# Optimization experiments

Hardware: AMD Instinct MI355X
Metric: run time of the kernel (lower is better)

## Reference

```python
import jax, jax.numpy as jnp
import numpy as np

L, D, H, DH, DI, V, S, B = 12, 768, 12, 64, 3072, 32000, 512, 2
LN_EPS = 1e-3  # keras LayerNormalization default epsilon

def _gelu(x):
    return x * 0.5 * (1.0 + jnp.tanh(np.sqrt(2.0 / np.pi).astype(np.float32) * (x + 0.044715 * x ** 3)))

def _layer_norm(x, g, b):
    mu = jnp.mean(x, axis=-1, keepdims=True)
    var = jnp.mean((x - mu) ** 2, axis=-1, keepdims=True)
    return (x - mu) * jax.lax.rsqrt(var + LN_EPS) * g + b

def _rel_shift(x, klen):
    # x: [qlen, rlen, b, n] -> shifted [qlen, klen, b, n]
    q, r, b, n = x.shape
    x = x.reshape(r, q, b, n)[1:].reshape(q, r - 1, b, n)
    return x[:, :klen]

def _pos_emb():
    # relative positions klen..-qlen+1 (attn_type='bi', mems=None -> klen=qlen=S)
    pos_seq = jnp.arange(S, -S, -1.0, dtype=jnp.float32)                      # [2S]
    inv_freq = 1.0 / (10000.0 ** (jnp.arange(0, D, 2, dtype=jnp.float32) / D))
    sinusoid = pos_seq[:, None] * inv_freq[None, :]
    pe = jnp.concatenate([jnp.sin(sinusoid), jnp.cos(sinusoid)], axis=-1)     # [2S, D]
    return jnp.broadcast_to(pe[:, None, :], (2 * S, B, D))                    # [2S, B, D]

def setup_inputs() -> dict:
    key = jax.random.key(0)
    ks = jax.random.split(key, 12)
    rn = lambda k, sh: 0.02 * jax.random.normal(k, sh, dtype=jnp.float32)
    return {
        "inp_k": jax.random.randint(ks[0], (S, B), 0, V),
        "seg_ids": jax.random.randint(ks[1], (S, B), 0, 2),
        "input_mask": jax.random.randint(ks[2], (S, B), 0, 2),
        "lookup_table": rn(ks[3], (V, D)),
        "Wq": rn(ks[4], (L, D, H, DH)),
        "Wk": rn(ks[5], (L, D, H, DH)),
        "Wv": rn(ks[6], (L, D, H, DH)),
        "Wr": rn(ks[7], (L, D, H, DH)),
        "Wo": rn(ks[8], (L, D, H, DH)),
        "r_w_bias": rn(ks[9], (L, H, DH)),
        "r_r_bias": rn(ks[10], (L, H, DH)),
        "r_s_bias": rn(ks[11], (L, H, DH)),
        "seg_embed": rn(jax.random.fold_in(key, 100), (L, 2, H, DH)),
        "ln_attn_g": jnp.ones((L, D), jnp.float32),
        "ln_attn_b": jnp.zeros((L, D), jnp.float32),
        "ln_ff_g": jnp.ones((L, D), jnp.float32),
        "ln_ff_b": jnp.zeros((L, D), jnp.float32),
        "ff_w1": rn(jax.random.fold_in(key, 101), (L, D, DI)),
        "ff_b1": jnp.zeros((L, DI), jnp.float32),
        "ff_w2": rn(jax.random.fold_in(key, 102), (L, DI, D)),
        "ff_b2": jnp.zeros((L, D), jnp.float32),
    }

def reference(inp_k, seg_ids, input_mask, lookup_table, Wq, Wk, Wv, Wr, Wo,
              r_w_bias, r_r_bias, r_s_bias, seg_embed,
              ln_attn_g, ln_attn_b, ln_ff_g, ln_ff_b,
              ff_w1, ff_b1, ff_w2, ff_b2):
    h = lookup_table[inp_k]                                                   # [S,B,D]
    r = _pos_emb()                                                            # [2S,B,D]
    # segment "same/different" one-hot matrix [q,k,b,2]
    seg_mat = jax.nn.one_hot((seg_ids[:, None, :] != seg_ids[None, :, :]).astype(jnp.int32), 2, dtype=jnp.float32)
    attn_mask = input_mask.astype(jnp.float32)[None, :, :, None]              # [1,S,B,1] broadcast over q,heads
    scale = DH ** -0.5
    for l in range(L):
        q = jnp.einsum('ibh,hnd->ibnd', h, Wq[l])
        k = jnp.einsum('ibh,hnd->ibnd', h, Wk[l])
        v = jnp.einsum('ibh,hnd->ibnd', h, Wv[l])
        kr = jnp.einsum('ibh,hnd->ibnd', r, Wr[l])                            # [2S,B,n,d]
        ac = jnp.einsum('ibnd,jbnd->ijbn', q + r_w_bias[l], k)
        bd = _rel_shift(jnp.einsum('ibnd,jbnd->ijbn', q + r_r_bias[l], kr), S)
        ef = jnp.einsum('ibnd,snd->ibns', q + r_s_bias[l], seg_embed[l])
        ef = jnp.einsum('ijbs,ibns->ijbn', seg_mat, ef)
        score = (ac + bd + ef) * scale - 1e30 * attn_mask
        prob = jax.nn.softmax(score, axis=1)                                  # softmax over key axis j
        vec = jnp.einsum('ijbn,jbnd->ibnd', prob, v)
        h = _layer_norm(jnp.einsum('ibnd,hnd->ibh', vec, Wo[l]) + h, ln_attn_g[l], ln_attn_b[l])
        ff = _gelu(jnp.einsum('ibd,df->ibf', h, ff_w1[l]) + ff_b1[l])
        ff = jnp.einsum('ibf,fd->ibd', ff, ff_w2[l]) + ff_b2[l]
        h = _layer_norm(ff + h, ln_ff_g[l], ln_ff_b[l])
    return h
```

## Files before the change

### kernel.cpp

```cpp
#include <hip/hip_runtime.h>
#include <hip/hip_bf16.h>
#include <math.h>

#define S 512
#define B 2
#define D 768
#define H 12
#define DH 64
#define DI 3072
#define NL 12
#define NTOK (S * B)

typedef __attribute__((ext_vector_type(8))) short short8v;
typedef __attribute__((ext_vector_type(4))) float f32x4;

__device__ __forceinline__ unsigned short f2b(float f) {
  union { float f; unsigned int u; } v; v.f = f;
  unsigned int r = v.u + 0x7fffu + ((v.u >> 16) & 1u);
  return (unsigned short)(r >> 16);
}
__device__ __forceinline__ float b2f(unsigned short u) {
  union { unsigned int u; float f; } v; v.u = ((unsigned int)u) << 16;
  return v.f;
}

__device__ __forceinline__ float gelu_f(float x) {
  const float c = 0.7978845608028654f;
  float t = tanhf(c * (x + 0.044715f * x * x * x));
  return x * 0.5f * (1.0f + t);
}

__device__ __forceinline__ int vkey(int r) {
  return (((r & 7) ^ ((r >> 3) & 7)) << 3);
}

__global__ __launch_bounds__(256) void embed_kernel(const int* __restrict__ inp_k,
                                                    const float* __restrict__ lut,
                                                    float* __restrict__ h,
                                                    unsigned short* __restrict__ h_bf) {
  int t = blockIdx.x;
  int id = inp_k[t];
  for (int j = threadIdx.x; j < D; j += 256) {
    float v = lut[(size_t)id * D + j];
    h[t * D + j] = v;
    h_bf[t * D + j] = f2b(v);
  }
}

__global__ __launch_bounds__(384) void posemb_kernel(unsigned short* __restrict__ r2b) {
  int j = blockIdx.x;
  int d = threadIdx.x;
  float pos = (float)(S - j);
  float inv_freq = expf(-logf(10000.0f) * (2.0f * (float)d / (float)D));
  float x = pos * inv_freq;
  r2b[j * D + d]       = f2b(sinf(x));
  r2b[j * D + 384 + d] = f2b(cosf(x));
}

__device__ __forceinline__ void transpose_swz(const float* __restrict__ src,
                                              unsigned short* __restrict__ dst,
                                              int K, int N, int tile, int n_base,
                                              unsigned short* __restrict__ Ls ) {
  int ntk = K >> 6;
  int tk = tile % ntk, tn = tile / ntk;
  int k0 = tk << 6, n0 = tn << 6;
  int tid = threadIdx.x;
  int kk = tid >> 4, c4 = (tid & 15) * 4;
#pragma unroll
  for (int r = 0; r < 4; ++r) {
    int k = kk + r * 16;
    float4 a = *(const float4*)&src[(size_t)(k0 + k) * N + n0 + c4];
    Ls[(c4 + 0) * 72 + k] = f2b(a.x);
    Ls[(c4 + 1) * 72 + k] = f2b(a.y);
    Ls[(c4 + 2) * 72 + k] = f2b(a.z);
    Ls[(c4 + 3) * 72 + k] = f2b(a.w);
  }
  __syncthreads();
  int nl = tid >> 2, kc0 = (tid & 3) << 4;
  int ng = n_base + n0;
  size_t tilebase = ((size_t)(ng >> 7) * ntk + tk) * 8192;
  int row = (ng & 64) + nl;
  int key = (row & 7) << 3;
  short8v v0 = *(short8v*)&Ls[nl * 72 + kc0];
  short8v v1 = *(short8v*)&Ls[nl * 72 + kc0 + 8];
  *(short8v*)&dst[tilebase + row * 64 + (kc0 ^ key)] = v0;
  *(short8v*)&dst[tilebase + row * 64 + ((kc0 + 8) ^ key)] = v1;
}

__global__ __launch_bounds__(256) void prep_all(const float* __restrict__ Wq,
                                                const float* __restrict__ Wk,
                                                const float* __restrict__ Wv,
                                                const float* __restrict__ Wr,
                                                const float* __restrict__ Wo,
                                                const float* __restrict__ W1,
                                                const float* __restrict__ W2,
                                                unsigned short* __restrict__ wqkv_t,
                                                unsigned short* __restrict__ wr_t,
                                                unsigned short* __restrict__ wo_t,
                                                unsigned short* __restrict__ w1_t,
                                                unsigned short* __restrict__ w2_t) {
  __shared__ __align__(16) unsigned short Ls[64 * 72];
  const size_t DD = (size_t)D * D;
  const size_t DDI = (size_t)D * DI;
  int tb = blockIdx.x;
  int l = tb / 1872, t2 = tb % 1872;
  int tid = threadIdx.x;
  if (t2 < 432) {
    int which = t2 / 144, tile = t2 % 144;
    const float* src = (which == 0 ? Wq : (which == 1 ? Wk : Wv)) + l * DD;
    transpose_swz(src, wqkv_t + l * 3 * DD, D, D, tile, which * D, Ls);
  } else if (t2 < 576) {
    transpose_swz(Wr + l * DD, wr_t + l * DD, D, D, t2 - 432, 0, Ls);
  } else if (t2 < 1152) {
    transpose_swz(W1 + l * DDI, w1_t + l * DDI, D, DI, t2 - 576, 0, Ls);
  } else if (t2 < 1728) {
    transpose_swz(W2 + l * DDI, w2_t + l * DDI, DI, D, t2 - 1152, 0, Ls);
  } else {
    int c = t2 - 1728;
    int tkk = c % 12, tnn = c / 12;
    int k0 = tkk << 6, n0 = tnn << 6;
    int nl = tid >> 2, kc0 = (tid & 3) << 4;
    const float* srcp = Wo + l * DD + (size_t)(n0 + nl) * D + k0 + kc0;
    float4 a0 = *(const float4*)&srcp[0];
    float4 a1 = *(const float4*)&srcp[4];
    float4 a2 = *(const float4*)&srcp[8];
    float4 a3 = *(const float4*)&srcp[12];
    short8v v0, v1;
    v0[0] = (short)f2b(a0.x); v0[1] = (short)f2b(a0.y); v0[2] = (short)f2b(a0.z); v0[3] = (short)f2b(a0.w);
    v0[4] = (short)f2b(a1.x); v0[5] = (short)f2b(a1.y); v0[6] = (short)f2b(a1.z); v0[7] = (short)f2b(a1.w);
    v1[0] = (short)f2b(a2.x); v1[1] = (short)f2b(a2.y); v1[2] = (short)f2b(a2.z); v1[3] = (short)f2b(a2.w);
    v1[4] = (short)f2b(a3.x); v1[5] = (short)f2b(a3.y); v1[6] = (short)f2b(a3.z); v1[7] = (short)f2b(a3.w);
    unsigned short* dst = wo_t + l * DD;
    size_t tilebase = ((size_t)(n0 >> 7) * 12 + tkk) * 8192;
    int row = (n0 & 64) + nl;
    int key = (row & 7) << 3;
    *(short8v*)&dst[tilebase + row * 64 + (kc0 ^ key)] = v0;
    *(short8v*)&dst[tilebase + row * 64 + ((kc0 + 8) ^ key)] = v1;
  }
}

template <int ACT, int OUTBF>
__device__ __forceinline__ void gemm_tile(const unsigned short* __restrict__ A,
                                          const unsigned short* __restrict__ Wt,
                                          const float* __restrict__ bias,
                                          float* __restrict__ Cf,
                                          unsigned short* __restrict__ Cb,
                                          int N, int K, int bm, int bn,
                                          int kbeg, int kend) {
  __shared__ __align__(16) unsigned short As[64 * 64];
  __shared__ __align__(16) unsigned short Bs[128 * 64];
  const int tid = threadIdx.x, lane = tid & 63, w = tid >> 6;
  const int l8 = lane >> 3, lm8 = lane & 7;
  const int aColByte = ((lm8 ^ l8) << 4);
  const int KT = K >> 6;
  const size_t wtn = (size_t)(bn >> 7) * KT;

  f32x4 acc[4][2];
#pragma unroll
  for (int mi = 0; mi < 4; ++mi)
#pragma unroll
    for (int ni = 0; ni < 2; ++ni)
      acc[mi][ni] = (f32x4){0.f, 0.f, 0.f, 0.f};

  for (int kt = kbeg; kt < kend; kt += 64) {
    __syncthreads();
#pragma unroll
    for (int c = 0; c < 2; ++c) {
      int row = c * 32 + w * 8 + l8;
      const char* src = (const char*)&A[(size_t)(bm + row) * K + kt] + aColByte;
      __builtin_amdgcn_global_load_lds(
          (const __attribute__((address_space(1))) void*)src,
          (__attribute__((address_space(3))) void*)((char*)As + c * 4096 + w * 1024),
          16, 0, 0);
    }
    const char* wt = (const char*)&Wt[(wtn + (kt >> 6)) * 8192];
#pragma unroll
    for (int c = 0; c < 4; ++c) {
      __builtin_amdgcn_global_load_lds(
          (const __attribute__((address_space(1))) void*)(wt + c * 4096 + w * 1024 + lane * 16),
          (__attribute__((address_space(3))) void*)((char*)Bs + c * 4096 + w * 1024),
          16, 0, 0);
    }
    __syncthreads();
#pragma unroll
    for (int ks = 0; ks < 2; ++ks) {
      const int kus = ks * 32 + (lane >> 4) * 8;
      short8v af[4], bf[2];
#pragma unroll
      for (int mi = 0; mi < 4; ++mi) {
        int row = mi * 16 + (lane & 15);
        af[mi] = *(const short8v*)&As[row * 64 + (kus ^ ((row & 7) << 3))];
      }
#pragma unroll
      for (int ni = 0; ni < 2; ++ni) {
        int row = w * 32 + ni * 16 + (lane & 15);
        bf[ni] = *(const short8v*)&Bs[row * 64 + (kus ^ ((row & 7) << 3))];
      }
#pragma unroll
      for (int mi = 0; mi < 4; ++mi)
#pragma unroll
        for (int ni = 0; ni < 2; ++ni)
          acc[mi][ni] = __builtin_amdgcn_mfma_f32_16x16x32_bf16(af[mi], bf[ni], acc[mi][ni], 0, 0, 0);
    }
  }

  int r0 = (lane >> 4) * 4, cc = lane & 15;
#pragma unroll
  for (int mi = 0; mi < 4; ++mi) {
    int row = bm + mi * 16 + r0;
#pragma unroll
    for (int ni = 0; ni < 2; ++ni) {
      int col = bn + w * 32 + ni * 16 + cc;
      float bv = bias ? bias[col] : 0.0f;
#pragma unroll
      for (int r = 0; r < 4; ++r) {
        float v = acc[mi][ni][r] + bv;
        if (ACT == 1) v = gelu_f(v);
        if (OUTBF) Cb[(size_t)(row + r) * N + col] = f2b(v);
        else       Cf[(size_t)(row + r) * N + col] = v;
      }
    }
  }
}

__global__ __launch_bounds__(256) void gemm_qkvkr(const unsigned short* __restrict__ h_bf,
                                                  const unsigned short* __restrict__ wqkv,
                                                  const unsigned short* __restrict__ r2_bf,
                                                  const unsigned short* __restrict__ wr,
                                                  unsigned short* __restrict__ qkv_bf,
                                                  unsigned short* __restrict__ kr_bf) {
  int bx = blockIdx.x;
  const unsigned short *A, *W;
  unsigned short* C;
  int N, bm, bn;
  if (bx < 288) {
    A = h_bf; W = wqkv; C = qkv_bf; N = 2304;
    bm = (bx / 18) * 64; bn = (bx % 18) * 128;
  } else {
    int b2 = bx - 288;
    A = r2_bf; W = wr; C = kr_bf; N = 768;
    bm = (b2 / 6) * 64; bn = (b2 % 6) * 128;
  }
  gemm_tile<0, 1>(A, W, nullptr, nullptr, C, N, 768, bm, bn, 0, 768);
}

template <int ACT>
__global__ __launch_bounds__(256) void gemm_bias(const unsigned short* __restrict__ A,
                                                 const unsigned short* __restrict__ W,
                                                 const float* __restrict__ bias,
                                                 unsigned short* __restrict__ C,
                                                 int N, int K, int ncb) {
  int bx = blockIdx.x;
  gemm_tile<ACT, 1>(A, W, bias, nullptr, C, N, K, (bx / ncb) * 64, (bx % ncb) * 128, 0, K);
}

__global__ __launch_bounds__(256) void gemm_splitk(const unsigned short* __restrict__ A,
                                                   const unsigned short* __restrict__ W,
                                                   float* __restrict__ part,
                                                   int N, int K, int kch) {
  int kz = blockIdx.z;
  float* Cf = part + (size_t)kz * NTOK * N;
  gemm_tile<0, 0>(A, W, nullptr, Cf, nullptr, N, K,
                  blockIdx.y * 64, blockIdx.x * 128, kz * kch, (kz + 1) * kch);
}

__global__ __launch_bounds__(256) void attn_kernel(const unsigned short* __restrict__ qkv,
                                                   const unsigned short* __restrict__ krb,
                                                   const int* __restrict__ seg_ids,
                                                   const int* __restrict__ input_mask,
                                                   const float* __restrict__ rwb,
                                                   const float* __restrict__ rrb,
                                                   const float* __restrict__ rsb,
                                                   const float* __restrict__ segemb,
                                                   unsigned short* __restrict__ vec_bf) {
  __shared__ __align__(16) char smem[64768];
  unsigned short* qw_s = (unsigned short*)(smem + 0);
  unsigned short* qr_s = (unsigned short*)(smem + 9216);
  unsigned short* k_s  = (unsigned short*)(smem + 18432);
  unsigned short* kr_s = (unsigned short*)(smem + 27648);
  unsigned short* bd_s = (unsigned short*)(smem + 46080);
  float* sc_s  = (float*)(smem + 18432);
  unsigned short* pb_s = (unsigned short*)(smem + 46080);
  unsigned short* vt_s = (unsigned short*)(smem + 54272);
  float* efs    = (float*)(smem + 63488);
  float* frow_s = (float*)(smem + 64000);
  float* rinv_s = (float*)(smem + 64256);
  int*   segrow = (int*)(smem + 64512);

  const int it = blockIdx.x * 64, b = blockIdx.y, n = blockIdx.z;
  const int tid = threadIdx.x, lane = tid & 63, w = tid >> 6;

  {
    int il = tid >> 2, d16 = (tid & 3) * 16;
    int t = (it + il) * B + b;
    short8v q0 = *(const short8v*)&qkv[(size_t)t * 2304 + n * 64 + d16];
    short8v q1 = *(const short8v*)&qkv[(size_t)t * 2304 + n * 64 + d16 + 8];
    short8v ow0, ow1, or0, or1;
#pragma unroll
    for (int e = 0; e < 8; ++e) {
      float f0 = b2f((unsigned short)q0[e]);
      float f1 = b2f((unsigned short)q1[e]);
      ow0[e] = (short)f2b(f0 + rwb[n * 64 + d16 + e]);
      ow1[e] = (short)f2b(f1 + rwb[n * 64 + d16 + 8 + e]);
      or0[e] = (short)f2b(f0 + rrb[n * 64 + d16 + e]);
      or1[e] = (short)f2b(f1 + rrb[n * 64 + d16 + 8 + e]);
    }
    *(short8v*)&qw_s[il * 72 + d16] = ow0;
    *(short8v*)&qw_s[il * 72 + d16 + 8] = ow1;
    *(short8v*)&qr_s[il * 72 + d16] = or0;
    *(short8v*)&qr_s[il * 72 + d16 + 8] = or1;
  }
  if (tid < 128) {
    int il = tid >> 1, s = tid & 1;
    int t = (it + il) * B + b;
    float acc = 0.0f;
    for (int d = 0; d < 64; ++d)
      acc = fmaf(b2f(qkv[(size_t)t * 2304 + n * 64 + d]) + rsb[n * 64 + d],
                 segemb[(s * H + n) * 64 + d], acc);
    efs[s * 64 + il] = acc;
  }
  if (tid < 64) segrow[tid] = seg_ids[(it + tid) * B + b];

  {
#pragma unroll
    for (int c = 0; c < 2; ++c) {
      int idx = tid + c * 256;
      int row = idx >> 3, k8 = (idx & 7) * 8;
      *(short8v*)&k_s[row * 72 + k8] =
          *(const short8v*)&qkv[(size_t)(row * B + b) * 2304 + 768 + n * 64 + k8];
    }
    int u0 = 448 - it;
#pragma unroll
    for (int c = 0; c < 4; ++c) {
      int idx = tid + c * 256;
      int row = idx >> 3, k8 = (idx & 7) * 8;
      *(short8v*)&kr_s[row * 72 + k8] =
          *(const short8v*)&krb[(size_t)(u0 + row) * 768 + n * 64 + k8];
    }
  }

  f32x4 acc_v[4];
#pragma unroll
  for (int mi = 0; mi < 4; ++mi) acc_v[mi] = (f32x4){0.f, 0.f, 0.f, 0.f};
  float m_run = -3.0e38f;
  float rsq = 0.0f;
  const int srow = tid >> 2, sc0 = (tid & 3) * 16;

  __syncthreads();

  for (int jt = 0; jt < 512; jt += 64) {
    const int vj = tid >> 2, vd16 = (tid & 3) * 16;
    short8v vl0 = *(const short8v*)&qkv[(size_t)((jt + vj) * B + b) * 2304 + 1536 + n * 64 + vd16];
    short8v vl1 = *(const short8v*)&qkv[(size_t)((jt + vj) * B + b) * 2304 + 1536 + n * 64 + vd16 + 8];

    f32x4 aac[4], abd[4][2];
#pragma unroll
    for (int mi = 0; mi < 4; ++mi) {
      aac[mi] = (f32x4){0.f, 0.f, 0.f, 0.f};
      abd[mi][0] = (f32x4){0.f, 0.f, 0.f, 0.f};
      abd[mi][1] = (f32x4){0.f, 0.f, 0.f, 0.f};
    }
#pragma unroll
    for (int ks = 0; ks < 2; ++ks) {
      int kb = ks * 32 + (lane >> 4) * 8;
      short8v aw[4], ar[4];
#pragma unroll
      for (int mi = 0; mi < 4; ++mi) {
        aw[mi] = *(const short8v*)&qw_s[(mi * 16 + (lane & 15)) * 72 + kb];
        ar[mi] = *(const short8v*)&qr_s[(mi * 16 + (lane & 15)) * 72 + kb];
      }
      short8v bk  = *(const short8v*)&k_s[(w * 16 + (lane & 15)) * 72 + kb];
      short8v br0 = *(const short8v*)&kr_s[(w * 32 + (lane & 15)) * 72 + kb];
      short8v br1 = *(const short8v*)&kr_s[(w * 32 + 16 + (lane & 15)) * 72 + kb];
#pragma unroll
      for (int mi = 0; mi < 4; ++mi) {
        aac[mi] = __builtin_amdgcn_mfma_f32_16x16x32_bf16(aw[mi], bk, aac[mi], 0, 0, 0);
        abd[mi][0] = __builtin_amdgcn_mfma_f32_16x16x32_bf16(ar[mi], br0, abd[mi][0], 0, 0, 0);
        abd[mi][1] = __builtin_amdgcn_mfma_f32_16x16x32_bf16(ar[mi], br1, abd[mi][1], 0, 0, 0);
      }
    }
#pragma unroll
    for (int mi = 0; mi < 4; ++mi)
#pragma unroll
      for (int ni = 0; ni < 2; ++ni)
#pragma unroll
        for (int r = 0; r < 4; ++r)
          bd_s[(mi * 16 + (lane >> 4) * 4 + r) * 136 + w * 32 + ni * 16 + (lane & 15)] =
              f2b(abd[mi][ni][r]);
    __syncthreads();

    {
      int jl = w * 16 + (lane & 15);
      int jg = jt + jl;
      float maskterm = -1e30f * (float)input_mask[jg * B + b];
      int segj = seg_ids[jg * B + b];
#pragma unroll
      for (int mi = 0; mi < 4; ++mi)
#pragma unroll
        for (int r = 0; r < 4; ++r) {
          int il = mi * 16 + (lane >> 4) * 4 + r;
          float bd = b2f(bd_s[il * 136 + 64 - il + jl]);
          float e = efs[(segrow[il] != segj ? 1 : 0) * 64 + il];
          sc_s[il * 68 + jl] = (aac[mi][r] + bd + e) * 0.125f + maskterm;
        }
    }
    __syncthreads();

    {
      float4 f0 = *(const float4*)&sc_s[srow * 68 + sc0];
      float4 f1 = *(const float4*)&sc_s[srow * 68 + sc0 + 4];
      float4 f2 = *(const float4*)&sc_s[srow * 68 + sc0 + 8];
      float4 f3 = *(const float4*)&sc_s[srow * 68 + sc0 + 12];
      float mx = fmaxf(fmaxf(fmaxf(f0.x, f0.y), fmaxf(f0.z, f0.w)),
                       fmaxf(fmaxf(f1.x, f1.y), fmaxf(f1.z, f1.w)));
      mx = fmaxf(mx, fmaxf(fmaxf(fmaxf(f2.x, f2.y), fmaxf(f2.z, f2.w)),
                           fmaxf(fmaxf(f3.x, f3.y), fmaxf(f3.z, f3.w))));
      mx = fmaxf(mx, __shfl_xor(mx, 1, 4));
      mx = fmaxf(mx, __shfl_xor(mx, 2, 4));
      float mnew = fmaxf(m_run, mx);
      float fsc = __expf(m_run - mnew);
      m_run = mnew;
      float p0 = __expf(f0.x - mnew), p1 = __expf(f0.y - mnew);
      float p2 = __expf(f0.z - mnew), p3 = __expf(f0.w - mnew);
      float p4 = __expf(f1.x - mnew), p5 = __expf(f1.y - mnew);
      float p6 = __expf(f1.z - mnew), p7 = __expf(f1.w - mnew);
      float p8 = __expf(f2.x - mnew), p9 = __expf(f2.y - mnew);
      float pa = __expf(f2.z - mnew), pb = __expf(f2.w - mnew);
      float pc = __expf(f3.x - mnew), pd = __expf(f3.y - mnew);
      float pe = __expf(f3.z - mnew), pf = __expf(f3.w - mnew);
      rsq = rsq * fsc + ((p0 + p1 + p2 + p3) + (p4 + p5 + p6 + p7)) +
                        ((p8 + p9 + pa + pb) + (pc + pd + pe + pf));
      short8v o0, o1;
      o0[0] = (short)f2b(p0); o0[1] = (short)f2b(p1); o0[2] = (short)f2b(p2); o0[3] = (short)f2b(p3);
      o0[4] = (short)f2b(p4); o0[5] = (short)f2b(p5); o0[6] = (short)f2b(p6); o0[7] = (short)f2b(p7);
      o1[0] = (short)f2b(p8); o1[1] = (short)f2b(p9); o1[2] = (short)f2b(pa); o1[3] = (short)f2b(pb);
      o1[4] = (short)f2b(pc); o1[5] = (short)f2b(pd); o1[6] = (short)f2b(pe); o1[7] = (short)f2b(pf);
      int key = vkey(srow);
      *(short8v*)&pb_s[srow * 64 + (sc0 ^ key)] = o0;
      *(short8v*)&pb_s[srow * 64 + ((sc0 + 8) ^ key)] = o1;
      if ((tid & 3) == 0) frow_s[srow] = fsc;
#pragma unroll
      for (int e = 0; e < 8; ++e) {
        int d0 = vd16 + e, d1 = vd16 + 8 + e;
        vt_s[d0 * 64 + (vj ^ vkey(d0))] = (unsigned short)vl0[e];
        vt_s[d1 * 64 + (vj ^ vkey(d1))] = (unsigned short)vl1[e];
      }
    }
    __syncthreads();

#pragma unroll
    for (int mi = 0; mi < 4; ++mi) {
#pragma unroll
      for (int r = 0; r < 4; ++r)
        acc_v[mi][r] *= frow_s[mi * 16 + (lane >> 4) * 4 + r];
    }
#pragma unroll
    for (int ks = 0; ks < 2; ++ks) {
      int kb = ks * 32 + (lane >> 4) * 8;
      int vrow = w * 16 + (lane & 15);
      short8v bv = *(const short8v*)&vt_s[vrow * 64 + (kb ^ vkey(vrow))];
#pragma unroll
      for (int mi = 0; mi < 4; ++mi) {
        int prow = mi * 16 + (lane & 15);
        short8v ap = *(const short8v*)&pb_s[prow * 64 + (kb ^ vkey(prow))];
        acc_v[mi] = __builtin_amdgcn_mfma_f32_16x16x32_bf16(ap, bv, acc_v[mi], 0, 0, 0);
      }
    }
    if (jt < 448) {
      int jn = jt + 64;
#pragma unroll
      for (int c = 0; c < 2; ++c) {
        int idx = tid + c * 256;
        int row = idx >> 3, k8 = (idx & 7) * 8;
        *(short8v*)&k_s[row * 72 + k8] =
            *(const short8v*)&qkv[(size_t)((jn + row) * B + b) * 2304 + 768 + n * 64 + k8];
      }
      int u0 = 448 - it + jn;
#pragma unroll
      for (int c = 0; c < 4; ++c) {
        int idx = tid + c * 256;
        int row = idx >> 3, k8 = (idx & 7) * 8;
        *(short8v*)&kr_s[row * 72 + k8] =
            *(const short8v*)&krb[(size_t)(u0 + row) * 768 + n * 64 + k8];
      }
    }
    __syncthreads();
  }

  {
    float tot = rsq;
    tot += __shfl_xor(tot, 1, 4);
    tot += __shfl_xor(tot, 2, 4);
    if ((tid & 3) == 0) rinv_s[srow] = 1.0f / tot;
  }
  __syncthreads();

#pragma unroll
  for (int mi = 0; mi < 4; ++mi)
#pragma unroll
    for (int r = 0; r < 4; ++r) {
      int row = mi * 16 + (lane >> 4) * 4 + r;
      int d = w * 16 + (lane & 15);
      int t = (it + row) * B + b;
      vec_bf[(size_t)t * D + n * 64 + d] = f2b(acc_v[mi][r] * rinv_s[row]);
    }
}

template <int P, int HASBIAS>
__global__ __launch_bounds__(256) void add_ln_reduce(const float* __restrict__ part,
                                                     const float* __restrict__ bias,
                                                     float* __restrict__ h,
                                                     unsigned short* __restrict__ h_bf,
                                                     const float* __restrict__ g,
                                                     const float* __restrict__ bi) {
  int t = blockIdx.x;
  int tid = threadIdx.x;
  __shared__ float red[256];
  float v[3];
  float s = 0.0f;
#pragma unroll
  for (int j = 0; j < 3; ++j) {
    int c = tid + j * 256;
    float x = 0.0f;
#pragma unroll
    for (int p = 0; p < P; ++p)
      x += part[(size_t)p * NTOK * D + (size_t)t * D + c];
    if (HASBIAS) x += bias[c];
    v[j] = x + h[(size_t)t * D + c];
    s += v[j];
  }
  red[tid] = s;
  __syncthreads();
  for (int st = 128; st > 0; st >>= 1) {
    if (tid < st) red[tid] += red[tid + st];
    __syncthreads();
  }
  float mu = red[0] / (float)D;
  __syncthreads();
  float s2 = 0.0f;
#pragma unroll
  for (int j = 0; j < 3; ++j) {
    float dd = v[j] - mu;
    s2 += dd * dd;
  }
  red[tid] = s2;
  __syncthreads();
  for (int st = 128; st > 0; st >>= 1) {
    if (tid < st) red[tid] += red[tid + st];
    __syncthreads();
  }
  float var = red[0] / (float)D;
  float rstd = rsqrtf(var + 1e-3f);
  __syncthreads();
#pragma unroll
  for (int j = 0; j < 3; ++j) {
    int c = tid + j * 256;
    float o = (v[j] - mu) * rstd * g[c] + bi[c];
    h[(size_t)t * D + c] = o;
    h_bf[(size_t)t * D + c] = f2b(o);
  }
}

extern "C" void kernel_launch(void* const* d_in, const int* in_sizes, int n_in,
                              void* d_out, int out_size, void* d_ws, size_t ws_size,
                              hipStream_t stream) {
  const int*   inp_k      = (const int*)d_in[0];
  const int*   seg_ids    = (const int*)d_in[1];
  const int*   input_mask = (const int*)d_in[2];
  const float* lut        = (const float*)d_in[3];
  const float* Wq         = (const float*)d_in[4];
  const float* Wk         = (const float*)d_in[5];
  const float* Wv         = (const float*)d_in[6];
  const float* Wr         = (const float*)d_in[7];
  const float* Wo         = (const float*)d_in[8];
  const float* r_w_bias   = (const float*)d_in[9];
  const float* r_r_bias   = (const float*)d_in[10];
  const float* r_s_bias   = (const float*)d_in[11];
  const float* seg_embed  = (const float*)d_in[12];
  const float* ln_attn_g  = (const float*)d_in[13];
  const float* ln_attn_b  = (const float*)d_in[14];
  const float* ln_ff_g    = (const float*)d_in[15];
  const float* ln_ff_b    = (const float*)d_in[16];
  const float* ff_w1      = (const float*)d_in[17];
  const float* ff_b1      = (const float*)d_in[18];
  const float* ff_w2      = (const float*)d_in[19];
  const float* ff_b2      = (const float*)d_in[20];

  float* h = (float*)d_out;
  char* wp = (char*)d_ws;
  auto alloc = [&](size_t bytes) -> void* {
    void* p = (void*)wp;
    wp += (bytes + 255) & ~(size_t)255;
    return p;
  };
  const size_t TOKD = (size_t)NTOK * D;
  const size_t DD = (size_t)D * D;
  const size_t DDI = (size_t)D * DI;
  unsigned short* qkv_bf = (unsigned short*)alloc((size_t)NTOK * 2304 * 2);
  unsigned short* kr_bf  = (unsigned short*)alloc(TOKD * 2);
  unsigned short* h_bf   = (unsigned short*)alloc(TOKD * 2);
  unsigned short* r2_bf  = (unsigned short*)alloc(TOKD * 2);
  unsigned short* vec_bf = (unsigned short*)alloc(TOKD * 2);
  unsigned short* ff1_bf = (unsigned short*)alloc((size_t)NTOK * DI * 2);
  float* part = (float*)alloc((size_t)4 * TOKD * 4);
  unsigned short* wqkv_t = (unsigned short*)alloc((size_t)NL * 3 * DD * 2);
  unsigned short* wr_t   = (unsigned short*)alloc((size_t)NL * DD * 2);
  unsigned short* wo_t   = (unsigned short*)alloc((size_t)NL * DD * 2);
  unsigned short* w1_t   = (unsigned short*)alloc((size_t)NL * DDI * 2);
  unsigned short* w2_t   = (unsigned short*)alloc((size_t)NL * DDI * 2);

  prep_all<<<NL * 1872, 256, 0, stream>>>(Wq, Wk, Wv, Wr, Wo, ff_w1, ff_w2,
                                          wqkv_t, wr_t, wo_t, w1_t, w2_t);
  embed_kernel<<<NTOK, 256, 0, stream>>>(inp_k, lut, h, h_bf);
  posemb_kernel<<<2 * S, 384, 0, stream>>>(r2_bf);

  for (int l = 0; l < NL; ++l) {
    gemm_qkvkr<<<384, 256, 0, stream>>>(h_bf, wqkv_t + (size_t)l * 3 * DD,
                                        r2_bf, wr_t + (size_t)l * DD,
                                        qkv_bf, kr_bf);

    attn_kernel<<<dim3(8, B, H), 256, 0, stream>>>(
        qkv_bf, kr_bf, seg_ids, input_mask,
        r_w_bias + (size_t)l * D, r_r_bias + (size_t)l * D,
        r_s_bias + (size_t)l * D, seg_embed + (size_t)l * 2 * H * DH,
        vec_bf);

    gemm_splitk<<<dim3(6, 16, 2), 256, 0, stream>>>(
        vec_bf, wo_t + (size_t)l * DD, part, D, D, 384);
    add_ln_reduce<2, 0><<<NTOK, 256, 0, stream>>>(
        part, nullptr, h, h_bf, ln_attn_g + (size_t)l * D, ln_attn_b + (size_t)l * D);

    gemm_bias<1><<<24 * 16, 256, 0, stream>>>(
        h_bf, w1_t + (size_t)l * DDI, ff_b1 + (size_t)l * DI, ff1_bf, DI, D, 24);

    gemm_splitk<<<dim3(6, 16, 4), 256, 0, stream>>>(
        ff1_bf, w2_t + (size_t)l * DDI, part, D, DI, 768);
    add_ln_reduce<4, 1><<<NTOK, 256, 0, stream>>>(
        part, ff_b2 + (size_t)l * D, h, h_bf, ln_ff_g + (size_t)l * D, ln_ff_b + (size_t)l * D);
  }
}
```

Measured before the change: 1.323 ms.

## Precompute kr for all layers, halve attention query tile, vectorize LayerNorm

The kr projection of the positional embedding does not depend on layer activations, so it moves out of the per-layer loop into one batched GEMM across all 12 layers, with kr stored for every layer. The attention kernel now uses 32-query tiles instead of 64, doubling the grid to 384 blocks for more occupancy, and shrinks the relative-shift band buffer and LDS to match. The add+LayerNorm reduce kernel now uses float4 loads and stores. The cost is extra workspace for kr across all layers, and each attention block reloads K/V for half as many queries.

```diff
diff --git a/kernel.cpp b/kernel.cpp
--- a/kernel.cpp
+++ b/kernel.cpp
@@ -31,7 +31,7 @@
 }
 
 __device__ __forceinline__ int vkey(int r) {
-  return (((r & 7) ^ ((r >> 3) & 7)) << 3);
+  return ((((r & 7) ^ ((r >> 3) & 7)) & 7) << 3);
 }
 
 __global__ __launch_bounds__(256) void embed_kernel(const int* __restrict__ inp_k,
@@ -223,25 +223,22 @@
   }
 }
 
-__global__ __launch_bounds__(256) void gemm_qkvkr(const unsigned short* __restrict__ h_bf,
-                                                  const unsigned short* __restrict__ wqkv,
-                                                  const unsigned short* __restrict__ r2_bf,
-                                                  const unsigned short* __restrict__ wr,
-                                                  unsigned short* __restrict__ qkv_bf,
-                                                  unsigned short* __restrict__ kr_bf) {
+__global__ __launch_bounds__(256) void gemm_qkv(const unsigned short* __restrict__ h_bf,
+                                                const unsigned short* __restrict__ wqkv,
+                                                unsigned short* __restrict__ qkv_bf) {
   int bx = blockIdx.x;
-  const unsigned short *A, *W;
-  unsigned short* C;
-  int N, bm, bn;
-  if (bx < 288) {
-    A = h_bf; W = wqkv; C = qkv_bf; N = 2304;
-    bm = (bx / 18) * 64; bn = (bx % 18) * 128;
-  } else {
-    int b2 = bx - 288;
-    A = r2_bf; W = wr; C = kr_bf; N = 768;
-    bm = (b2 / 6) * 64; bn = (b2 % 6) * 128;
-  }
-  gemm_tile<0, 1>(A, W, nullptr, nullptr, C, N, 768, bm, bn, 0, 768);
+  gemm_tile<0, 1>(h_bf, wqkv, nullptr, nullptr, qkv_bf, 2304, 768,
+                  (bx / 18) * 64, (bx % 18) * 128, 0, 768);
+}
+
+__global__ __launch_bounds__(256) void gemm_kr_all(const unsigned short* __restrict__ r2_bf,
+                                                   const unsigned short* __restrict__ wr_t,
+                                                   unsigned short* __restrict__ kr_all) {
+  int bx = blockIdx.x;
+  int l = bx / 96, b2 = bx % 96;
+  gemm_tile<0, 1>(r2_bf, wr_t + (size_t)l * D * D, nullptr, nullptr,
+                  kr_all + (size_t)l * NTOK * D, 768, 768,
+                  (b2 / 6) * 64, (b2 % 6) * 128, 0, 768);
 }
 
 template <int ACT>
@@ -273,53 +270,47 @@
                                                    const float* __restrict__ rsb,
                                                    const float* __restrict__ segemb,
                                                    unsigned short* __restrict__ vec_bf) {
-  __shared__ __align__(16) char smem[64768];
+  __shared__ __align__(16) char smem[51840];
   unsigned short* qw_s = (unsigned short*)(smem + 0);
-  unsigned short* qr_s = (unsigned short*)(smem + 9216);
-  unsigned short* k_s  = (unsigned short*)(smem + 18432);
-  unsigned short* kr_s = (unsigned short*)(smem + 27648);
-  unsigned short* bd_s = (unsigned short*)(smem + 46080);
-  float* sc_s  = (float*)(smem + 18432);
-  unsigned short* pb_s = (unsigned short*)(smem + 46080);
-  unsigned short* vt_s = (unsigned short*)(smem + 54272);
-  float* efs    = (float*)(smem + 63488);
-  float* frow_s = (float*)(smem + 64000);
-  float* rinv_s = (float*)(smem + 64256);
-  int*   segrow = (int*)(smem + 64512);
-
-  const int it = blockIdx.x * 64, b = blockIdx.y, n = blockIdx.z;
+  unsigned short* qr_s = (unsigned short*)(smem + 4608);
+  unsigned short* k_s  = (unsigned short*)(smem + 9216);
+  unsigned short* kr_s = (unsigned short*)(smem + 18432);
+  unsigned short* bd_s = (unsigned short*)(smem + 32256);
+  unsigned short* vt_s = (unsigned short*)(smem + 38912);
+  unsigned short* pb_s = (unsigned short*)(smem + 47104);
+  float* sc_s  = (float*)(smem + 9216);
+  float* efs    = (float*)(smem + 51200);
+  float* frow_s = (float*)(smem + 51456);
+  float* rinv_s = (float*)(smem + 51584);
+  int*   segrow = (int*)(smem + 51712);
+
+  const int it = blockIdx.x * 32, b = blockIdx.y, n = blockIdx.z;
   const int tid = threadIdx.x, lane = tid & 63, w = tid >> 6;
 
   {
-    int il = tid >> 2, d16 = (tid & 3) * 16;
+    int il = tid >> 3, d8 = (tid & 7) * 8;
     int t = (it + il) * B + b;
-    short8v q0 = *(const short8v*)&qkv[(size_t)t * 2304 + n * 64 + d16];
-    short8v q1 = *(const short8v*)&qkv[(size_t)t * 2304 + n * 64 + d16 + 8];
-    short8v ow0, ow1, or0, or1;
+    short8v q0 = *(const short8v*)&qkv[(size_t)t * 2304 + n * 64 + d8];
+    short8v ow0, or0;
 #pragma unroll
     for (int e = 0; e < 8; ++e) {
       float f0 = b2f((unsigned short)q0[e]);
-      float f1 = b2f((unsigned short)q1[e]);
-      ow0[e] = (short)f2b(f0 + rwb[n * 64 + d16 + e]);
-      ow1[e] = (short)f2b(f1 + rwb[n * 64 + d16 + 8 + e]);
-      or0[e] = (short)f2b(f0 + rrb[n * 64 + d16 + e]);
-      or1[e] = (short)f2b(f1 + rrb[n * 64 + d16 + 8 + e]);
-    }
-    *(short8v*)&qw_s[il * 72 + d16] = ow0;
-    *(short8v*)&qw_s[il * 72 + d16 + 8] = ow1;
-    *(short8v*)&qr_s[il * 72 + d16] = or0;
-    *(short8v*)&qr_s[il * 72 + d16 + 8] = or1;
-  }
-  if (tid < 128) {
+      ow0[e] = (short)f2b(f0 + rwb[n * 64 + d8 + e]);
+      or0[e] = (short)f2b(f0 + rrb[n * 64 + d8 + e]);
+    }
+    *(short8v*)&qw_s[il * 72 + d8] = ow0;
+    *(short8v*)&qr_s[il * 72 + d8] = or0;
+  }
+  if (tid < 64) {
     int il = tid >> 1, s = tid & 1;
     int t = (it + il) * B + b;
     float acc = 0.0f;
     for (int d = 0; d < 64; ++d)
       acc = fmaf(b2f(qkv[(size_t)t * 2304 + n * 64 + d]) + rsb[n * 64 + d],
                  segemb[(s * H + n) * 64 + d], acc);
-    efs[s * 64 + il] = acc;
-  }
-  if (tid < 64) segrow[tid] = seg_ids[(it + tid) * B + b];
+    efs[s * 32 + il] = acc;
+  }
+  if (tid < 32) segrow[tid] = seg_ids[(it + tid) * B + b];
 
   {
 #pragma unroll
@@ -329,9 +320,9 @@
       *(short8v*)&k_s[row * 72 + k8] =
           *(const short8v*)&qkv[(size_t)(row * B + b) * 2304 + 768 + n * 64 + k8];
     }
-    int u0 = 448 - it;
-#pragma unroll
-    for (int c = 0; c < 4; ++c) {
+    int u0 = 481 - it;
+#pragma unroll
+    for (int c = 0; c < 3; ++c) {
       int idx = tid + c * 256;
       int row = idx >> 3, k8 = (idx & 7) * 8;
       *(short8v*)&kr_s[row * 72 + k8] =
@@ -339,12 +330,12 @@
     }
   }
 
-  f32x4 acc_v[4];
-#pragma unroll
-  for (int mi = 0; mi < 4; ++mi) acc_v[mi] = (f32x4){0.f, 0.f, 0.f, 0.f};
+  f32x4 acc_v[2];
+  acc_v[0] = (f32x4){0.f, 0.f, 0.f, 0.f};
+  acc_v[1] = (f32x4){0.f, 0.f, 0.f, 0.f};
   float m_run = -3.0e38f;
   float rsq = 0.0f;
-  const int srow = tid >> 2, sc0 = (tid & 3) * 16;
+  const int srow = tid >> 3, sc0 = (tid & 7) * 8;
 
   __syncthreads();
 
@@ -353,40 +344,49 @@
     short8v vl0 = *(const short8v*)&qkv[(size_t)((jt + vj) * B + b) * 2304 + 1536 + n * 64 + vd16];
     short8v vl1 = *(const short8v*)&qkv[(size_t)((jt + vj) * B + b) * 2304 + 1536 + n * 64 + vd16 + 8];
 
-    f32x4 aac[4], abd[4][2];
-#pragma unroll
-    for (int mi = 0; mi < 4; ++mi) {
-      aac[mi] = (f32x4){0.f, 0.f, 0.f, 0.f};
-      abd[mi][0] = (f32x4){0.f, 0.f, 0.f, 0.f};
-      abd[mi][1] = (f32x4){0.f, 0.f, 0.f, 0.f};
+    f32x4 jacc[3][2];
+#pragma unroll
+    for (int t = 0; t < 3; ++t) {
+      jacc[t][0] = (f32x4){0.f, 0.f, 0.f, 0.f};
+      jacc[t][1] = (f32x4){0.f, 0.f, 0.f, 0.f};
     }
 #pragma unroll
     for (int ks = 0; ks < 2; ++ks) {
       int kb = ks * 32 + (lane >> 4) * 8;
-      short8v aw[4], ar[4];
-#pragma unroll
-      for (int mi = 0; mi < 4; ++mi) {
+      short8v aw[2], ar[2];
+#pragma unroll
+      for (int mi = 0; mi < 2; ++mi) {
         aw[mi] = *(const short8v*)&qw_s[(mi * 16 + (lane & 15)) * 72 + kb];
         ar[mi] = *(const short8v*)&qr_s[(mi * 16 + (lane & 15)) * 72 + kb];
       }
-      short8v bk  = *(const short8v*)&k_s[(w * 16 + (lane & 15)) * 72 + kb];
-      short8v br0 = *(const short8v*)&kr_s[(w * 32 + (lane & 15)) * 72 + kb];
-      short8v br1 = *(const short8v*)&kr_s[(w * 32 + 16 + (lane & 15)) * 72 + kb];
-#pragma unroll
-      for (int mi = 0; mi < 4; ++mi) {
-        aac[mi] = __builtin_amdgcn_mfma_f32_16x16x32_bf16(aw[mi], bk, aac[mi], 0, 0, 0);
-        abd[mi][0] = __builtin_amdgcn_mfma_f32_16x16x32_bf16(ar[mi], br0, abd[mi][0], 0, 0, 0);
-        abd[mi][1] = __builtin_amdgcn_mfma_f32_16x16x32_bf16(ar[mi], br1, abd[mi][1], 0, 0, 0);
-      }
-    }
-#pragma unroll
-    for (int mi = 0; mi < 4; ++mi)
-#pragma unroll
-      for (int ni = 0; ni < 2; ++ni)
-#pragma unroll
-        for (int r = 0; r < 4; ++r)
-          bd_s[(mi * 16 + (lane >> 4) * 4 + r) * 136 + w * 32 + ni * 16 + (lane & 15)] =
-              f2b(abd[mi][ni][r]);
+      {
+        short8v bk = *(const short8v*)&k_s[(w * 16 + (lane & 15)) * 72 + kb];
+        jacc[0][0] = __builtin_amdgcn_mfma_f32_16x16x32_bf16(aw[0], bk, jacc[0][0], 0, 0, 0);
+        jacc[0][1] = __builtin_amdgcn_mfma_f32_16x16x32_bf16(aw[1], bk, jacc[0][1], 0, 0, 0);
+      }
+      {
+        short8v br = *(const short8v*)&kr_s[(w * 16 + (lane & 15)) * 72 + kb];
+        jacc[1][0] = __builtin_amdgcn_mfma_f32_16x16x32_bf16(ar[0], br, jacc[1][0], 0, 0, 0);
+        jacc[1][1] = __builtin_amdgcn_mfma_f32_16x16x32_bf16(ar[1], br, jacc[1][1], 0, 0, 0);
+      }
+      if (w < 2) {
+        short8v br = *(const short8v*)&kr_s[((w + 4) * 16 + (lane & 15)) * 72 + kb];
+        jacc[2][0] = __builtin_amdgcn_mfma_f32_16x16x32_bf16(ar[0], br, jacc[2][0], 0, 0, 0);
+        jacc[2][1] = __builtin_amdgcn_mfma_f32_16x16x32_bf16(ar[1], br, jacc[2][1], 0, 0, 0);
+      }
+    }
+#pragma unroll
+    for (int t = 1; t < 3; ++t) {
+      int cf = w + (t - 1) * 4;
+      if (t == 1 || w < 2) {
+#pragma unroll
+        for (int mi = 0; mi < 2; ++mi)
+#pragma unroll
+          for (int r = 0; r < 4; ++r)
+            bd_s[(mi * 16 + (lane >> 4) * 4 + r) * 104 + cf * 16 + (lane & 15)] =
+                f2b(jacc[t][mi][r]);
+      }
+    }
     __syncthreads();
 
     {
@@ -395,13 +395,13 @@
       float maskterm = -1e30f * (float)input_mask[jg * B + b];
       int segj = seg_ids[jg * B + b];
 #pragma unroll
-      for (int mi = 0; mi < 4; ++mi)
+      for (int mi = 0; mi < 2; ++mi)
 #pragma unroll
         for (int r = 0; r < 4; ++r) {
           int il = mi * 16 + (lane >> 4) * 4 + r;
-          float bd = b2f(bd_s[il * 136 + 64 - il + jl]);
-          float e = efs[(segrow[il] != segj ? 1 : 0) * 64 + il];
-          sc_s[il * 68 + jl] = (aac[mi][r] + bd + e) * 0.125f + maskterm;
+          float bd = b2f(bd_s[il * 104 + 31 - il + jl]);
+          float e = efs[(segrow[il] != segj ? 1 : 0) * 32 + il];
+          sc_s[il * 68 + jl] = (jacc[0][mi][r] + bd + e) * 0.125f + maskterm;
         }
     }
     __syncthreads();
@@ -409,14 +409,11 @@
     {
       float4 f0 = *(const float4*)&sc_s[srow * 68 + sc0];
       float4 f1 = *(const float4*)&sc_s[srow * 68 + sc0 + 4];
-      float4 f2 = *(const float4*)&sc_s[srow * 68 + sc0 + 8];
-      float4 f3 = *(const float4*)&sc_s[srow * 68 + sc0 + 12];
       float mx = fmaxf(fmaxf(fmaxf(f0.x, f0.y), fmaxf(f0.z, f0.w)),
                        fmaxf(fmaxf(f1.x, f1.y), fmaxf(f1.z, f1.w)));
-      mx = fmaxf(mx, fmaxf(fmaxf(fmaxf(f2.x, f2.y), fmaxf(f2.z, f2.w)),
-                           fmaxf(fmaxf(f3.x, f3.y), fmaxf(f3.z, f3.w))));
-      mx = fmaxf(mx, __shfl_xor(mx, 1, 4));
-      mx = fmaxf(mx, __shfl_xor(mx, 2, 4));
+      mx = fmaxf(mx, __shfl_xor(mx, 1, 8));
+      mx = fmaxf(mx, __shfl_xor(mx, 2, 8));
+      mx = fmaxf(mx, __shfl_xor(mx, 4, 8));
       float mnew = fmaxf(m_run, mx);
       float fsc = __expf(m_run - mnew);
       m_run = mnew;
@@ -424,21 +421,12 @@
       float p2 = __expf(f0.z - mnew), p3 = __expf(f0.w - mnew);
       float p4 = __expf(f1.x - mnew), p5 = __expf(f1.y - mnew);
       float p6 = __expf(f1.z - mnew), p7 = __expf(f1.w - mnew);
-      float p8 = __expf(f2.x - mnew), p9 = __expf(f2.y - mnew);
-      float pa = __expf(f2.z - mnew), pb = __expf(f2.w - mnew);
-      float pc = __expf(f3.x - mnew), pd = __expf(f3.y - mnew);
-      float pe = __expf(f3.z - mnew), pf = __expf(f3.w - mnew);
-      rsq = rsq * fsc + ((p0 + p1 + p2 + p3) + (p4 + p5 + p6 + p7)) +
-                        ((p8 + p9 + pa + pb) + (pc + pd + pe + pf));
-      short8v o0, o1;
+      rsq = rsq * fsc + ((p0 + p1 + p2 + p3) + (p4 + p5 + p6 + p7));
+      short8v o0;
       o0[0] = (short)f2b(p0); o0[1] = (short)f2b(p1); o0[2] = (short)f2b(p2); o0[3] = (short)f2b(p3);
       o0[4] = (short)f2b(p4); o0[5] = (short)f2b(p5); o0[6] = (short)f2b(p6); o0[7] = (short)f2b(p7);
-      o1[0] = (short)f2b(p8); o1[1] = (short)f2b(p9); o1[2] = (short)f2b(pa); o1[3] = (short)f2b(pb);
-      o1[4] = (short)f2b(pc); o1[5] = (short)f2b(pd); o1[6] = (short)f2b(pe); o1[7] = (short)f2b(pf);
-      int key = vkey(srow);
-      *(short8v*)&pb_s[srow * 64 + (sc0 ^ key)] = o0;
-      *(short8v*)&pb_s[srow * 64 + ((sc0 + 8) ^ key)] = o1;
-      if ((tid & 3) == 0) frow_s[srow] = fsc;
+      *(short8v*)&pb_s[srow * 64 + (sc0 ^ vkey(srow))] = o0;
+      if ((tid & 7) == 0) frow_s[srow] = fsc;
 #pragma unroll
       for (int e = 0; e < 8; ++e) {
         int d0 = vd16 + e, d1 = vd16 + 8 + e;
@@ -449,7 +437,7 @@
     __syncthreads();
 
 #pragma unroll
-    for (int mi = 0; mi < 4; ++mi) {
+    for (int mi = 0; mi < 2; ++mi) {
 #pragma unroll
       for (int r = 0; r < 4; ++r)
         acc_v[mi][r] *= frow_s[mi * 16 + (lane >> 4) * 4 + r];
@@ -460,7 +448,7 @@
       int vrow = w * 16 + (lane & 15);
       short8v bv = *(const short8v*)&vt_s[vrow * 64 + (kb ^ vkey(vrow))];
 #pragma unroll
-      for (int mi = 0; mi < 4; ++mi) {
+      for (int mi = 0; mi < 2; ++mi) {
         int prow = mi * 16 + (lane & 15);
         short8v ap = *(const short8v*)&pb_s[prow * 64 + (kb ^ vkey(prow))];
         acc_v[mi] = __builtin_amdgcn_mfma_f32_16x16x32_bf16(ap, bv, acc_v[mi], 0, 0, 0);
@@ -475,9 +463,9 @@
         *(short8v*)&k_s[row * 72 + k8] =
             *(const short8v*)&qkv[(size_t)((jn + row) * B + b) * 2304 + 768 + n * 64 + k8];
       }
-      int u0 = 448 - it + jn;
-#pragma unroll
-      for (int c = 0; c < 4; ++c) {
+      int u0 = 481 - it + jn;
+#pragma unroll
+      for (int c = 0; c < 3; ++c) {
         int idx = tid + c * 256;
         int row = idx >> 3, k8 = (idx & 7) * 8;
         *(short8v*)&kr_s[row * 72 + k8] =
@@ -489,14 +477,15 @@
 
   {
     float tot = rsq;
-    tot += __shfl_xor(tot, 1, 4);
-    tot += __shfl_xor(tot, 2, 4);
-    if ((tid & 3) == 0) rinv_s[srow] = 1.0f / tot;
+    tot += __shfl_xor(tot, 1, 8);
+    tot += __shfl_xor(tot, 2, 8);
+    tot += __shfl_xor(tot, 4, 8);
+    if ((tid & 7) == 0) rinv_s[srow] = 1.0f / tot;
   }
   __syncthreads();
 
 #pragma unroll
-  for (int mi = 0; mi < 4; ++mi)
+  for (int mi = 0; mi < 2; ++mi)
 #pragma unroll
     for (int r = 0; r < 4; ++r) {
       int row = mi * 16 + (lane >> 4) * 4 + r;
@@ -516,18 +505,23 @@
   int t = blockIdx.x;
   int tid = threadIdx.x;
   __shared__ float red[256];
-  float v[3];
+  float vx = 0.f, vy = 0.f, vz = 0.f, vw = 0.f;
   float s = 0.0f;
-#pragma unroll
-  for (int j = 0; j < 3; ++j) {
-    int c = tid + j * 256;
-    float x = 0.0f;
-#pragma unroll
-    for (int p = 0; p < P; ++p)
-      x += part[(size_t)p * NTOK * D + (size_t)t * D + c];
-    if (HASBIAS) x += bias[c];
-    v[j] = x + h[(size_t)t * D + c];
-    s += v[j];
+  int c = tid * 4;
+  if (tid < 192) {
+    float4 x = {0.f, 0.f, 0.f, 0.f};
+#pragma unroll
+    for (int p = 0; p < P; ++p) {
+      float4 pp = *(const float4*)&part[(size_t)p * NTOK * D + (size_t)t * D + c];
+      x.x += pp.x; x.y += pp.y; x.z += pp.z; x.w += pp.w;
+    }
+    if (HASBIAS) {
+      float4 bb = *(const float4*)&bias[c];
+      x.x += bb.x; x.y += bb.y; x.z += bb.z; x.w += bb.w;
+    }
+    float4 hh = *(const float4*)&h[(size_t)t * D + c];
+    vx = x.x + hh.x; vy = x.y + hh.y; vz = x.z + hh.z; vw = x.w + hh.w;
+    s = vx + vy + vz + vw;
   }
   red[tid] = s;
   __syncthreads();
@@ -538,10 +532,9 @@
   float mu = red[0] / (float)D;
   __syncthreads();
   float s2 = 0.0f;
-#pragma unroll
-  for (int j = 0; j < 3; ++j) {
-    float dd = v[j] - mu;
-    s2 += dd * dd;
+  if (tid < 192) {
+    float dx = vx - mu, dy = vy - mu, dz = vz - mu, dw = vw - mu;
+    s2 = dx * dx + dy * dy + dz * dz + dw * dw;
   }
   red[tid] = s2;
   __syncthreads();
@@ -552,12 +545,18 @@
   float var = red[0] / (float)D;
   float rstd = rsqrtf(var + 1e-3f);
   __syncthreads();
-#pragma unroll
-  for (int j = 0; j < 3; ++j) {
-    int c = tid + j * 256;
-    float o = (v[j] - mu) * rstd * g[c] + bi[c];
-    h[(size_t)t * D + c] = o;
-    h_bf[(size_t)t * D + c] = f2b(o);
+  if (tid < 192) {
+    float4 gg = *(const float4*)&g[c];
+    float4 bb = *(const float4*)&bi[c];
+    float o0 = (vx - mu) * rstd * gg.x + bb.x;
+    float o1 = (vy - mu) * rstd * gg.y + bb.y;
+    float o2 = (vz - mu) * rstd * gg.z + bb.z;
+    float o3 = (vw - mu) * rstd * gg.w + bb.w;
+    float4 of = {o0, o1, o2, o3};
+    *(float4*)&h[(size_t)t * D + c] = of;
+    ushort4 ob;
+    ob.x = f2b(o0); ob.y = f2b(o1); ob.z = f2b(o2); ob.w = f2b(o3);
+    *(ushort4*)&h_bf[(size_t)t * D + c] = ob;
   }
 }
 
@@ -597,7 +596,7 @@
   const size_t DD = (size_t)D * D;
   const size_t DDI = (size_t)D * DI;
   unsigned short* qkv_bf = (unsigned short*)alloc((size_t)NTOK * 2304 * 2);
-  unsigned short* kr_bf  = (unsigned short*)alloc(TOKD * 2);
+  unsigned short* kr_all = (unsigned short*)alloc((size_t)NL * TOKD * 2);
   unsigned short* h_bf   = (unsigned short*)alloc(TOKD * 2);
   unsigned short* r2_bf  = (unsigned short*)alloc(TOKD * 2);
   unsigned short* vec_bf = (unsigned short*)alloc(TOKD * 2);
@@ -613,14 +612,13 @@
                                           wqkv_t, wr_t, wo_t, w1_t, w2_t);
   embed_kernel<<<NTOK, 256, 0, stream>>>(inp_k, lut, h, h_bf);
   posemb_kernel<<<2 * S, 384, 0, stream>>>(r2_bf);
+  gemm_kr_all<<<NL * 96, 256, 0, stream>>>(r2_bf, wr_t, kr_all);
 
   for (int l = 0; l < NL; ++l) {
-    gemm_qkvkr<<<384, 256, 0, stream>>>(h_bf, wqkv_t + (size_t)l * 3 * DD,
-                                        r2_bf, wr_t + (size_t)l * DD,
-                                        qkv_bf, kr_bf);
-
-    attn_kernel<<<dim3(8, B, H), 256, 0, stream>>>(
-        qkv_bf, kr_bf, seg_ids, input_mask,
+    gemm_qkv<<<288, 256, 0, stream>>>(h_bf, wqkv_t + (size_t)l * 3 * DD, qkv_bf);
+
+    attn_kernel<<<dim3(16, B, H), 256, 0, stream>>>(
+        qkv_bf, kr_all + (size_t)l * TOKD, seg_ids, input_mask,
         r_w_bias + (size_t)l * D, r_r_bias + (size_t)l * D,
         r_s_bias + (size_t)l * D, seg_embed + (size_t)l * 2 * H * DH,
         vec_bf);
```

New measurement: 1.300 ms. Within noise of the previous version (-1.8%).
